# Kernel optimization log

Hardware: AMD Instinct MI355X
Metric: run time of the kernel (lower is better)

## Reference

```python
import jax, jax.numpy as jnp
import numpy as np

D_STATE = 16
D_CONV = 4


def layer_norm(x, g, b, eps=1e-5):
    mu = jnp.mean(x, axis=-1, keepdims=True)
    var = jnp.mean(jnp.square(x - mu), axis=-1, keepdims=True)
    return (x - mu) * jax.lax.rsqrt(var + eps) * g + b


def silu(x):
    return x * jax.nn.sigmoid(x)


def mamba(x, in_w, conv_w, conv_b, xproj_w, dt_w, dt_b, Alog, Dp, out_w):
    # x: [B, L, d_model]; in_w: [2*di, d_model]; conv_w: [di, d_conv]
    Bsz, L, _ = x.shape
    di = Dp.shape[0]
    xz = jnp.einsum('bld,ed->ble', x, in_w)          # [B,L,2*di]
    xs, z = jnp.split(xz, 2, axis=-1)
    # causal depthwise conv over L
    xt = xs.transpose(0, 2, 1)                        # [B,di,L]
    xt = jax.lax.conv_general_dilated(
        xt, conv_w[:, None, :], (1,), [(D_CONV - 1, 0)],
        feature_group_count=di, dimension_numbers=('NCH', 'OIH', 'NCH'))
    xs = silu((xt + conv_b[None, :, None]).transpose(0, 2, 1))  # [B,L,di]
    # input-dependent dt, B, C
    dbl = jnp.einsum('bld,ed->ble', xs, xproj_w)      # [B,L,dt_rank+2*ds]
    dt_rank = dt_w.shape[1]
    dt, Bc, Cc = jnp.split(dbl, [dt_rank, dt_rank + D_STATE], axis=-1)
    dt = jax.nn.softplus(jnp.einsum('blr,dr->bld', dt, dt_w) + dt_b)  # [B,L,di]
    A = -jnp.exp(Alog)                                # [di,ds]
    dA = jnp.exp(dt[..., None] * A)                   # [B,L,di,ds]
    dBx = dt[..., None] * Bc[:, :, None, :] * xs[..., None]  # [B,L,di,ds]

    def step(h, inp):
        dA_t, dBx_t, C_t = inp                        # [B,di,ds],[B,di,ds],[B,ds]
        h = dA_t * h + dBx_t
        y = jnp.einsum('bds,bs->bd', h, C_t)
        return h, y

    h0 = jnp.zeros((Bsz, di, D_STATE), x.dtype)
    _, ys = jax.lax.scan(step, h0, (dA.transpose(1, 0, 2, 3),
                                    dBx.transpose(1, 0, 2, 3),
                                    Cc.transpose(1, 0, 2)))
    y = ys.transpose(1, 0, 2) + Dp * xs               # [B,L,di]
    y = y * silu(z)
    return jnp.einsum('bld,od->blo', y, out_w)        # [B,L,d_model]


def _make_mamba_params(key, d_model, scale=0.02):
    di = 2 * d_model
    dt_rank = (d_model + 15) // 16
    ks = jax.random.split(key, 7)
    in_w = jax.random.normal(ks[0], (2 * di, d_model), jnp.float32) * scale
    conv_w = jax.random.normal(ks[1], (di, D_CONV), jnp.float32) * scale
    conv_b = jnp.zeros((di,), jnp.float32)
    xproj_w = jax.random.normal(ks[2], (dt_rank + 2 * D_STATE, di), jnp.float32) * scale
    dt_w = jax.random.normal(ks[3], (di, dt_rank), jnp.float32) * scale
    dt_b = jax.random.uniform(ks[4], (di,), jnp.float32, -5.0, -2.0)
    Alog = jnp.log(jnp.tile(jnp.arange(1, D_STATE + 1, dtype=jnp.float32), (di, 1)))
    Dp = jnp.ones((di,), jnp.float32)
    out_w = jax.random.normal(ks[5], (d_model, di), jnp.float32) * scale
    return in_w, conv_w, conv_b, xproj_w, dt_w, dt_b, Alog, Dp, out_w


def setup_inputs() -> dict:
    key = jax.random.key(0)
    B, L, D = 4, 2048, 1024
    DFF = 4 * D
    ks = jax.random.split(key, 8)
    x = jax.random.normal(ks[0], (B, L, D), jnp.float32)
    m1 = _make_mamba_params(ks[1], D)
    m2 = _make_mamba_params(ks[2], D)
    names1 = ['m1_in_w', 'm1_conv_w', 'm1_conv_b', 'm1_xproj_w', 'm1_dt_w', 'm1_dt_b', 'm1_Alog', 'm1_D', 'm1_out_w']
    names2 = ['m2_in_w', 'm2_conv_w', 'm2_conv_b', 'm2_xproj_w', 'm2_dt_w', 'm2_dt_b', 'm2_Alog', 'm2_D', 'm2_out_w']
    inp = {'x': x}
    inp.update(dict(zip(names1, m1)))
    inp.update(dict(zip(names2, m2)))
    inp['norm_g'] = jnp.ones((D,), jnp.float32)
    inp['norm_b'] = jnp.zeros((D,), jnp.float32)
    inp['ffn_g'] = jnp.ones((D,), jnp.float32)
    inp['ffn_b'] = jnp.zeros((D,), jnp.float32)
    inp['ff1_w'] = jax.random.normal(ks[3], (DFF, D), jnp.float32) * 0.02
    inp['ff1_b'] = jnp.zeros((DFF,), jnp.float32)
    inp['ff2_w'] = jax.random.normal(ks[4], (D, DFF), jnp.float32) * 0.02
    inp['ff2_b'] = jnp.zeros((D,), jnp.float32)
    return inp


def reference(x,
              m1_in_w, m1_conv_w, m1_conv_b, m1_xproj_w, m1_dt_w, m1_dt_b, m1_Alog, m1_D, m1_out_w,
              m2_in_w, m2_conv_w, m2_conv_b, m2_xproj_w, m2_dt_w, m2_dt_b, m2_Alog, m2_D, m2_out_w,
              norm_g, norm_b, ffn_g, ffn_b, ff1_w, ff1_b, ff2_w, ff2_b):
    # BiDirectionalAddBlock (dropout/droppath = identity in eval)
    h = layer_norm(x, norm_g, norm_b)
    fwd = mamba(h, m1_in_w, m1_conv_w, m1_conv_b, m1_xproj_w, m1_dt_w, m1_dt_b, m1_Alog, m1_D, m1_out_w)
    bwd = mamba(h[:, ::-1], m2_in_w, m2_conv_w, m2_conv_b, m2_xproj_w, m2_dt_w, m2_dt_b, m2_Alog, m2_D, m2_out_w)
    block_out = jax.nn.gelu(fwd + bwd + x, approximate=False)  # note: original does NOT flip bwd back
    x = x + block_out
    # FeedForward
    hf = layer_norm(x, ffn_g, ffn_b)
    hf = jax.nn.gelu(jnp.einsum('bld,hd->blh', hf, ff1_w) + ff1_b, approximate=False)
    x = x + jnp.einsum('blh,dh->bld', hf, ff2_w) + ff2_b
    return x
```

## Files before the change

### kernel.cpp

```cpp
#include <hip/hip_runtime.h>
#include <cmath>


namespace {

using u16 = unsigned short;
using uint = unsigned int;

constexpr int kB = 4;
constexpr int kL = 2048;
constexpr int kD = 1024;
constexpr int kDI = 2048;
constexpr int kDFF = 4096;
constexpr int kDS = 16;
constexpr int kDtRank = 64;
constexpr int kNPad = 128;
constexpr int kM = kB * kL;
constexpr int kNCH = 64;

typedef short bf16x8 __attribute__((ext_vector_type(8)));
typedef float f32x4  __attribute__((ext_vector_type(4)));
typedef unsigned short ushort8 __attribute__((ext_vector_type(8)));

__device__ __forceinline__ float bf2f(u16 u) {
  union { unsigned int i; float f; } c; c.i = ((unsigned int)u) << 16; return c.f;
}
__device__ __forceinline__ u16 f2bf(float f) {
  union { float f; unsigned int i; } c; c.f = f;
  return (u16)((c.i + 0x7FFFu + ((c.i >> 16) & 1u)) >> 16);
}
__device__ __forceinline__ float geluf(float v) {
  return 0.5f * v * (1.f + erff(v * 0.70710678118654752f));
}
__device__ __forceinline__ float softplusf(float v) {
  return (v > 0.f) ? (v + log1pf(__expf(-v))) : log1pf(__expf(v));
}
__device__ __forceinline__ float siluf(float v) {
  return v / (1.f + __expf(-v));
}
__device__ __forceinline__ float exp2_fast(float v) {
  return __builtin_amdgcn_exp2f(v);
}
__device__ __forceinline__ float softplus_fast(float v) {
  const float a = __builtin_fabsf(v);
  const float e = exp2_fast(-a * 1.44269504088896f);
  const float l = __log2f(1.f + e) * 0.69314718055995f;
  return fmaxf(v, 0.f) + l;
}

__device__ __forceinline__ void async16(const u16* g, u16* l) {
  __builtin_amdgcn_global_load_lds(
      (const __attribute__((address_space(1))) uint*)g,
      (__attribute__((address_space(3))) uint*)l, 16, 0, 0);
}

__global__ __launch_bounds__(256) void ln_kernel(
    const float* __restrict__ x, const float* __restrict__ g,
    const float* __restrict__ b, u16* __restrict__ out) {
  const int row = blockIdx.x;
  const int tid = threadIdx.x;
  const float4 v = ((const float4*)(x + (size_t)row * kD))[tid];
  float s  = v.x + v.y + v.z + v.w;
  float ss = v.x * v.x + v.y * v.y + v.z * v.z + v.w * v.w;
  #pragma unroll
  for (int off = 32; off; off >>= 1) {
    s  += __shfl_xor(s, off);
    ss += __shfl_xor(ss, off);
  }
  __shared__ float ls[4], lss[4];
  const int wid = tid >> 6;
  if ((tid & 63) == 0) { ls[wid] = s; lss[wid] = ss; }
  __syncthreads();
  s  = ls[0] + ls[1] + ls[2] + ls[3];
  ss = lss[0] + lss[1] + lss[2] + lss[3];
  const float mu  = s * (1.f / kD);
  const float inv = rsqrtf(ss * (1.f / kD) - mu * mu + 1e-5f);
  const float4 gg = ((const float4*)g)[tid];
  const float4 bb = ((const float4*)b)[tid];
  ushort4 o;
  o.x = f2bf((v.x - mu) * inv * gg.x + bb.x);
  o.y = f2bf((v.y - mu) * inv * gg.y + bb.y);
  o.z = f2bf((v.z - mu) * inv * gg.z + bb.z);
  o.w = f2bf((v.w - mu) * inv * gg.w + bb.w);
  ((ushort4*)(out + (size_t)row * kD))[tid] = o;
}

__global__ __launch_bounds__(256) void combine_ln_kernel(
    const float* __restrict__ x, float* __restrict__ out,
    const float* __restrict__ g, const float* __restrict__ b,
    u16* __restrict__ h) {
  const int row = blockIdx.x;
  const int tid = threadIdx.x;
  const float4 xv = ((const float4*)(x + (size_t)row * kD))[tid];
  const float4 bv = ((const float4*)(out + (size_t)row * kD))[tid];
  float4 o;
  o.x = xv.x + geluf(bv.x + xv.x);
  o.y = xv.y + geluf(bv.y + xv.y);
  o.z = xv.z + geluf(bv.z + xv.z);
  o.w = xv.w + geluf(bv.w + xv.w);
  ((float4*)(out + (size_t)row * kD))[tid] = o;
  float s  = o.x + o.y + o.z + o.w;
  float ss = o.x * o.x + o.y * o.y + o.z * o.z + o.w * o.w;
  #pragma unroll
  for (int off = 32; off; off >>= 1) {
    s  += __shfl_xor(s, off);
    ss += __shfl_xor(ss, off);
  }
  __shared__ float ls[4], lss[4];
  const int wid = tid >> 6;
  if ((tid & 63) == 0) { ls[wid] = s; lss[wid] = ss; }
  __syncthreads();
  s  = ls[0] + ls[1] + ls[2] + ls[3];
  ss = lss[0] + lss[1] + lss[2] + lss[3];
  const float mu  = s * (1.f / kD);
  const float inv = rsqrtf(ss * (1.f / kD) - mu * mu + 1e-5f);
  const float4 gg = ((const float4*)g)[tid];
  const float4 bb = ((const float4*)b)[tid];
  ushort4 ho;
  ho.x = f2bf((o.x - mu) * inv * gg.x + bb.x);
  ho.y = f2bf((o.y - mu) * inv * gg.y + bb.y);
  ho.z = f2bf((o.z - mu) * inv * gg.z + bb.z);
  ho.w = f2bf((o.w - mu) * inv * gg.w + bb.w);
  ((ushort4*)(h + (size_t)row * kD))[tid] = ho;
}

struct KJob { const float* s; u16* d; int n4; int blk0; int xp; };
struct KJobs { KJob j[10]; };

__global__ __launch_bounds__(256) void cvt_all_kernel(KJobs J) {
  const int bi = blockIdx.x;
  #pragma unroll
  for (int k = 0; k < 10; k++) {
    const KJob job = J.j[k];
    const int nb = (job.n4 + 255) >> 8;
    if (bi >= job.blk0 && bi < job.blk0 + nb) {
      const int i = (bi - job.blk0) * 256 + threadIdx.x;
      if (i < job.n4) {
        ushort4 o = {0, 0, 0, 0};
        bool valid = true;
        if (job.xp) valid = ((i * 4) >> 11) < (kDtRank + 2 * kDS);
        if (valid) {
          const float4 v = ((const float4*)job.s)[i];
          o.x = f2bf(v.x); o.y = f2bf(v.y); o.z = f2bf(v.z); o.w = f2bf(v.w);
        }
        ((ushort4*)job.d)[i] = o;
      }
      return;
    }
  }
}

template <int TILEN, int ACT, bool BIAS, bool ACC, bool OUTBF, bool REV,
          bool AMAP, bool CMAP>
__global__ __launch_bounds__(256) void gemm_mfma(
    const u16* __restrict__ A, int lda,
    const u16* __restrict__ W, int ldw,
    void* __restrict__ Cp, int ldc, int K,
    const float* __restrict__ bias, int seg_len, int row_off) {
  constexpr int MI = (TILEN == 128) ? 4 : 2;
  constexpr int WSTR = TILEN / 32;
  __shared__ __align__(16) u16 As[128][64];
  __shared__ __align__(16) u16 Ws[TILEN][64];
  const int tid  = threadIdx.x;
  const int bm   = blockIdx.x * 128;
  const int bn   = blockIdx.y * TILEN;
  const int lane = tid & 63;
  const int wv   = tid >> 6;
  const int wm   = (TILEN == 128) ? (wv >> 1) * 64 : wv * 32;
  const int wn   = (TILEN == 128) ? (wv & 1) * 64 : 0;
  const int l15  = lane & 15;
  const int quad = lane >> 4;
  const int srow = lane >> 3;
  const int swz  = ((lane & 7) ^ srow) * 8;
  const int jx   = (l15 & 7) * 16;

  int ab = 0, all0 = bm;
  if (AMAP || CMAP) {
    ab = bm / seg_len;
    all0 = bm - ab * seg_len;
  }

  int arowv[4];
  #pragma unroll
  for (int it = 0; it < 4; it++) {
    const int rl = it * 32 + wv * 8 + srow;
    if (AMAP) {
      arowv[it] = REV ? (ab * kL + kL - 1 - row_off - all0 - rl)
                      : (ab * kL + row_off + all0 + rl);
    } else {
      arowv[it] = bm + rl;
    }
  }

  f32x4 acc[MI][4];
  #pragma unroll
  for (int i = 0; i < MI; i++)
    #pragma unroll
    for (int j = 0; j < 4; j++) acc[i][j] = (f32x4){0.f, 0.f, 0.f, 0.f};

  for (int k0 = 0; k0 < K; k0 += 64) {
    #pragma unroll
    for (int it = 0; it < 4; it++) {
      const int rl = it * 32 + wv * 8 + srow;
      async16(A + (size_t)arowv[it] * lda + k0 + swz, &As[it * 32 + wv * 8][0]);
    }
    #pragma unroll
    for (int it = 0; it < WSTR; it++) {
      const int rl = it * 32 + wv * 8 + srow;
      async16(W + (size_t)(bn + rl) * ldw + k0 + swz, &Ws[it * 32 + wv * 8][0]);
    }
    __syncthreads();
    #pragma unroll
    for (int ks = 0; ks < 64; ks += 32) {
      const int cb = ((ks >> 3) + quad) * 16;
      bf16x8 af[MI], wf[4];
      #pragma unroll
      for (int i = 0; i < MI; i++)
        af[i] = *(const bf16x8*)((const char*)&As[wm + i * 16 + l15][0] +
                                 (cb ^ jx));
      #pragma unroll
      for (int j = 0; j < 4; j++)
        wf[j] = *(const bf16x8*)((const char*)&Ws[wn + j * 16 + l15][0] +
                                 (cb ^ jx));
      #pragma unroll
      for (int i = 0; i < MI; i++)
        #pragma unroll
        for (int j = 0; j < 4; j++)
          acc[i][j] = __builtin_amdgcn_mfma_f32_16x16x32_bf16(
              af[i], wf[j], acc[i][j], 0, 0, 0);
    }
    __syncthreads();
  }

  #pragma unroll
  for (int i = 0; i < MI; i++) {
    #pragma unroll
    for (int j = 0; j < 4; j++) {
      const int col = bn + wn + j * 16 + l15;
      #pragma unroll
      for (int r = 0; r < 4; r++) {
        const int rl2 = wm + i * 16 + quad * 4 + r;
        const int crow = CMAP ? (ab * kL + row_off + all0 + rl2) : (bm + rl2);
        float v = acc[i][j][r];
        if (BIAS) v += bias[col];
        if (ACT == 1) v = softplusf(v);
        if (ACT == 2) v = geluf(v);
        if (OUTBF) {
          ((u16*)Cp)[(size_t)crow * ldc + col] = f2bf(v);
        } else {
          float* p = (float*)Cp + (size_t)crow * ldc + col;
          if (ACC) *p = *p + v; else *p = v;
        }
      }
    }
  }
}

__global__ __launch_bounds__(256) void dt_kernel(
    const u16* __restrict__ dbl, const u16* __restrict__ wdt,
    const float* __restrict__ bias, u16* __restrict__ dtb) {
  __shared__ __align__(16) u16 sh[2][128][64];
  const int tid  = threadIdx.x;
  const int bm   = blockIdx.x * 128;
  const int bn   = blockIdx.y * 128;
  const int lane = tid & 63;
  const int wv   = tid >> 6;
  const int wm   = (wv >> 1) * 64;
  const int wn   = (wv & 1) * 64;
  const int l15  = lane & 15;
  const int quad = lane >> 4;
  const int srow = lane >> 3;
  const int swz  = ((lane & 7) ^ srow) * 8;
  const int jx   = (l15 & 7) * 16;

  #pragma unroll
  for (int it = 0; it < 4; it++) {
    const int rl = it * 32 + wv * 8 + srow;
    async16(dbl + (size_t)(bm + rl) * kNPad + swz, &sh[0][it * 32 + wv * 8][0]);
    async16(wdt + (size_t)(bn + rl) * kDtRank + swz,
            &sh[1][it * 32 + wv * 8][0]);
  }
  __syncthreads();

  f32x4 acc[4][4];
  #pragma unroll
  for (int i = 0; i < 4; i++)
    #pragma unroll
    for (int j = 0; j < 4; j++) acc[i][j] = (f32x4){0.f, 0.f, 0.f, 0.f};

  #pragma unroll
  for (int ks = 0; ks < 2; ks++) {
    const int cb = (ks * 4 + quad) * 16;
    bf16x8 af[4], wf[4];
    #pragma unroll
    for (int i = 0; i < 4; i++)
      af[i] = *(const bf16x8*)((const char*)&sh[0][wm + i * 16 + l15][0] +
                               (cb ^ jx));
    #pragma unroll
    for (int j = 0; j < 4; j++)
      wf[j] = *(const bf16x8*)((const char*)&sh[1][wn + j * 16 + l15][0] +
                               (cb ^ jx));
    #pragma unroll
    for (int i = 0; i < 4; i++)
      #pragma unroll
      for (int j = 0; j < 4; j++)
        acc[i][j] = __builtin_amdgcn_mfma_f32_16x16x32_bf16(
            af[i], wf[j], acc[i][j], 0, 0, 0);
  }
  __syncthreads();

  u16* C = &sh[0][0][0];
  #pragma unroll
  for (int i = 0; i < 4; i++) {
    #pragma unroll
    for (int j = 0; j < 4; j++) {
      const int colL = wn + j * 16 + l15;
      const float bv = bias[bn + colL];
      #pragma unroll
      for (int r = 0; r < 4; r++) {
        const int rl2 = wm + i * 16 + quad * 4 + r;
        C[rl2 * 128 + colL] = f2bf(softplus_fast(acc[i][j][r] + bv));
      }
    }
  }
  __syncthreads();

  #pragma unroll
  for (int i = 0; i < 8; i++) {
    const int cidx = i * 256 + tid;
    const int row  = cidx >> 4;
    const int cin  = (cidx & 15) * 8;
    const ushort8 val = *(const ushort8*)&C[row * 128 + cin];
    *(ushort8*)&dtb[(size_t)(bm + row) * kDI + bn + cin] = val;
  }
}

__global__ __launch_bounds__(256) void conv_silu_kernel(
    const u16* __restrict__ xz, const float* __restrict__ w,
    const float* __restrict__ cb, u16* __restrict__ xs,
    const u16* __restrict__ tail_in, u16* __restrict__ tail_out,
    int seg_len, int row_off) {
  const int t = blockIdx.x * 256 + threadIdx.x;
  const int c = t & (kDI - 1);
  const int r = t >> 11;
  const int b = r / seg_len;
  const int ll = r - b * seg_len;
  const int tpos = row_off + ll;

  const float xv0 = bf2f(xz[(size_t)r * (2 * kDI) + c]);
  float acc = cb[c] + w[c * 4 + 3] * xv0;
  #pragma unroll
  for (int j = 1; j <= 3; j++) {
    if (tpos - j >= 0) {
      float xp;
      if (ll - j >= 0) {
        xp = bf2f(xz[(size_t)(r - j) * (2 * kDI) + c]);
      } else {
        xp = bf2f(tail_in[(b * 3 + (3 + ll - j)) * kDI + c]);
      }
      acc += w[c * 4 + 3 - j] * xp;
    }
  }
  xs[(size_t)r * kDI + c] = f2bf(siluf(acc));
  if (ll >= seg_len - 3) {
    tail_out[(b * 3 + (ll - (seg_len - 3))) * kDI + c] = f2bf(xv0);
  }
}

__global__ __launch_bounds__(256, 8) void scan_phaseA(
    const u16* __restrict__ dt, const u16* __restrict__ xs,
    const u16* __restrict__ dbl, const float* __restrict__ Alog,
    float* __restrict__ Pbuf, float* __restrict__ Hbuf,
    int Lseg, int Lc) {
  __shared__ float Bls[32][16];
  const int tid = threadIdx.x;
  const int c = blockIdx.x * 256 + tid;
  const int k = blockIdx.y;
  const int b = blockIdx.z;
  const int base = b * Lseg + k * Lc;
  for (int idx = tid; idx < Lc * 16; idx += 256) {
    const int r = idx >> 4, j = idx & 15;
    Bls[r][j] = bf2f(dbl[(size_t)(base + r) * kNPad + kDtRank + j]);
  }
  __syncthreads();
  float Ac[16], h[16];
  float dtsum = 0.f;
  #pragma unroll
  for (int s = 0; s < 16; s++) {
    Ac[s] = -__expf(Alog[c * kDS + s]) * 1.44269504088896f;
    h[s] = 0.f;
  }
  for (int r = 0; r < Lc; r++) {
    const size_t row = (size_t)(base + r);
    const float dtv = bf2f(dt[row * kDI + c]);
    const float dtx = dtv * bf2f(xs[row * kDI + c]);
    dtsum += dtv;
    const float4* Brow = (const float4*)Bls[r];
    #pragma unroll
    for (int s4 = 0; s4 < 4; s4++) {
      const float4 Bv = Brow[s4];
      const float bb[4] = {Bv.x, Bv.y, Bv.z, Bv.w};
      #pragma unroll
      for (int q = 0; q < 4; q++) {
        const int s = s4 * 4 + q;
        const float dA = exp2_fast(dtv * Ac[s]);
        h[s] = dA * h[s] + dtx * bb[q];
      }
    }
  }
  const size_t o = (((size_t)b * kNCH + k) * kDI + c) * 16;
  #pragma unroll
  for (int s4 = 0; s4 < 4; s4++) {
    *(float4*)&Pbuf[o + s4 * 4] =
        make_float4(exp2_fast(Ac[s4 * 4 + 0] * dtsum),
                    exp2_fast(Ac[s4 * 4 + 1] * dtsum),
                    exp2_fast(Ac[s4 * 4 + 2] * dtsum),
                    exp2_fast(Ac[s4 * 4 + 3] * dtsum));
    *(float4*)&Hbuf[o + s4 * 4] =
        make_float4(h[s4 * 4], h[s4 * 4 + 1], h[s4 * 4 + 2], h[s4 * 4 + 3]);
  }
}

__global__ __launch_bounds__(256) void scan_phaseB(
    float* __restrict__ Pbuf, const float* __restrict__ Hbuf,
    float* __restrict__ hstate, int first) {
  const int t = blockIdx.x * 256 + threadIdx.x;
  const int s = t & 15;
  const int c = (t >> 4) & (kDI - 1);
  const int b = t >> 15;
  float cur = first ? 0.f : hstate[t];
  for (int k = 0; k < kNCH; k++) {
    const size_t idx = (((size_t)b * kNCH + k) * kDI + c) * 16 + s;
    const float p = Pbuf[idx];
    const float hl = Hbuf[idx];
    Pbuf[idx] = cur;
    cur = p * cur + hl;
  }
  hstate[t] = cur;
}

__global__ __launch_bounds__(256, 8) void scan_phaseC(
    const u16* __restrict__ dt, u16* __restrict__ xs,
    const u16* __restrict__ dbl, const u16* __restrict__ xz,
    const float* __restrict__ Alog, const float* __restrict__ Dp,
    const float* __restrict__ Pbuf, int Lseg, int Lc) {
  __shared__ float BC[32][32];
  const int tid = threadIdx.x;
  const int c = blockIdx.x * 256 + tid;
  const int k = blockIdx.y;
  const int b = blockIdx.z;
  const int base = b * Lseg + k * Lc;
  for (int idx = tid; idx < Lc * 32; idx += 256) {
    const int r = idx >> 5, j = idx & 31;
    BC[r][j] = bf2f(dbl[(size_t)(base + r) * kNPad + kDtRank + j]);
  }
  __syncthreads();
  float Ac[16], h[16];
  const size_t o = (((size_t)b * kNCH + k) * kDI + c) * 16;
  #pragma unroll
  for (int s4 = 0; s4 < 4; s4++) {
    const float4 hv = *(const float4*)&Pbuf[o + s4 * 4];
    h[s4 * 4 + 0] = hv.x; h[s4 * 4 + 1] = hv.y;
    h[s4 * 4 + 2] = hv.z; h[s4 * 4 + 3] = hv.w;
  }
  #pragma unroll
  for (int s = 0; s < 16; s++)
    Ac[s] = -__expf(Alog[c * kDS + s]) * 1.44269504088896f;
  const float Dv = Dp[c];
  for (int r = 0; r < Lc; r++) {
    const size_t row = (size_t)(base + r);
    const float dtv = bf2f(dt[row * kDI + c]);
    const float xv = bf2f(xs[row * kDI + c]);
    const float dtx = dtv * xv;
    float y = 0.f;
    const float4* Brow = (const float4*)BC[r];
    const float4* Crow = (const float4*)&BC[r][16];
    #pragma unroll
    for (int s4 = 0; s4 < 4; s4++) {
      const float4 Bv = Brow[s4];
      const float4 Cv = Crow[s4];
      const float bb[4] = {Bv.x, Bv.y, Bv.z, Bv.w};
      const float cc[4] = {Cv.x, Cv.y, Cv.z, Cv.w};
      #pragma unroll
      for (int q = 0; q < 4; q++) {
        const int s = s4 * 4 + q;
        const float dA = exp2_fast(dtv * Ac[s]);
        h[s] = dA * h[s] + dtx * bb[q];
        y += h[s] * cc[q];
      }
    }
    const float z = bf2f(xz[row * (2 * kDI) + kDI + c]);
    xs[row * kDI + c] = f2bf((y + Dv * xv) * siluf(z));
  }
}

}

extern "C" void kernel_launch(void* const* d_in, const int* in_sizes, int n_in,
                              void* d_out, int out_size, void* d_ws,
                              size_t ws_size, hipStream_t stream) {
  const float* x = (const float*)d_in[0];
  const float* in_w[2]    = {(const float*)d_in[1],  (const float*)d_in[10]};
  const float* conv_w[2]  = {(const float*)d_in[2],  (const float*)d_in[11]};
  const float* conv_b[2]  = {(const float*)d_in[3],  (const float*)d_in[12]};
  const float* xproj_w[2] = {(const float*)d_in[4],  (const float*)d_in[13]};
  const float* dt_w[2]    = {(const float*)d_in[5],  (const float*)d_in[14]};
  const float* dt_b[2]    = {(const float*)d_in[6],  (const float*)d_in[15]};
  const float* Alog[2]    = {(const float*)d_in[7],  (const float*)d_in[16]};
  const float* Dp[2]      = {(const float*)d_in[8],  (const float*)d_in[17]};
  const float* out_w[2]   = {(const float*)d_in[9],  (const float*)d_in[18]};
  const float* norm_g = (const float*)d_in[19];
  const float* norm_b = (const float*)d_in[20];
  const float* ffn_g  = (const float*)d_in[21];
  const float* ffn_b  = (const float*)d_in[22];
  const float* ff1_w  = (const float*)d_in[23];
  const float* ff1_b  = (const float*)d_in[24];
  const float* ff2_w  = (const float*)d_in[25];
  const float* ff2_b  = (const float*)d_in[26];
  float* out = (float*)d_out;

  constexpr size_t kWCache =
      2 * ((size_t)4096 * kD + (size_t)kD * kDI + (size_t)kNPad * kDI +
           (size_t)kDI * kDtRank) * 2 +
      ((size_t)kDFF * kD + (size_t)kD * kDFF) * 2;
  auto need = [](int nseg) -> size_t {
    const size_t mseg = (size_t)kM / nseg;
    size_t sz = kWCache + 4096;
    sz += (size_t)kM * kD * 2;
    sz += mseg * 4096 * 2;
    sz += mseg * 2048 * 2;
    sz += mseg * 128 * 2;
    sz += mseg * 2048 * 2;
    sz += 2 * (size_t)kB * kNCH * kDI * kDS * 4;
    sz += (size_t)kB * kDI * kDS * 4;
    sz += 2 * (size_t)kB * 3 * kDI * 2;
    sz += 32 * 256;
    return sz;
  };
  int nseg = 1;
  while (nseg <= 16 && need(nseg) > ws_size) nseg *= 2;
  if (nseg > 16) return;
  const int Lseg = kL / nseg;
  const int Mseg = kM / nseg;
  const int Lc = Lseg / kNCH;

  char* base = (char*)d_ws;
  size_t off = 0;
  auto alloc = [&](size_t bytes) {
    char* p = base + off;
    off = (off + bytes + 255) & ~(size_t)255;
    return p;
  };
  u16* w_in[2], *w_out[2], *w_xp[2], *w_dt[2];
  for (int m = 0; m < 2; m++) {
    w_in[m]  = (u16*)alloc((size_t)4096 * kD * 2);
    w_out[m] = (u16*)alloc((size_t)kD * kDI * 2);
    w_xp[m]  = (u16*)alloc((size_t)kNPad * kDI * 2);
    w_dt[m]  = (u16*)alloc((size_t)kDI * kDtRank * 2);
  }
  u16* w_f1 = (u16*)alloc((size_t)kDFF * kD * 2);
  u16* w_f2 = (u16*)alloc((size_t)kD * kDFF * 2);
  u16*   h      = (u16*)alloc((size_t)kM * kD * 2);
  u16*   xz     = (u16*)alloc((size_t)Mseg * 4096 * 2);
  u16*   xs     = (u16*)alloc((size_t)Mseg * 2048 * 2);
  u16*   dbl    = (u16*)alloc((size_t)Mseg * 128 * 2);
  u16*   dtb    = (u16*)alloc((size_t)Mseg * 2048 * 2);
  float* Pbuf   = (float*)alloc((size_t)kB * kNCH * kDI * kDS * 4);
  float* Hbuf   = (float*)alloc((size_t)kB * kNCH * kDI * kDS * 4);
  float* hstate = (float*)alloc((size_t)kB * kDI * kDS * 4);
  u16*   tail0  = (u16*)alloc((size_t)kB * 3 * kDI * 2);
  u16*   tail1  = (u16*)alloc((size_t)kB * 3 * kDI * 2);

  {
    KJobs J;
    int b = 0, ji = 0;
    auto addjob = [&](const float* s, u16* d, int n4, int xp) {
      J.j[ji].s = s; J.j[ji].d = d; J.j[ji].n4 = n4;
      J.j[ji].blk0 = b; J.j[ji].xp = xp;
      b += (n4 + 255) >> 8;
      ji++;
    };
    for (int m = 0; m < 2; m++) {
      addjob(in_w[m],  w_in[m],  (4096 * kD) / 4, 0);
      addjob(out_w[m], w_out[m], (kD * kDI) / 4, 0);
      addjob(xproj_w[m], w_xp[m], (kNPad * kDI) / 4, 1);
      addjob(dt_w[m],  w_dt[m],  (kDI * kDtRank) / 4, 0);
    }
    addjob(ff1_w, w_f1, (kDFF * kD) / 4, 0);
    addjob(ff2_w, w_f2, (kD * kDFF) / 4, 0);
    cvt_all_kernel<<<b, 256, 0, stream>>>(J);
  }

  ln_kernel<<<kM, 256, 0, stream>>>(x, norm_g, norm_b, h);

  for (int m = 0; m < 2; m++) {
    for (int s = 0; s < nseg; s++) {
      const int l0 = s * Lseg;
      u16* tin  = (s & 1) ? tail0 : tail1;
      u16* tout = (s & 1) ? tail1 : tail0;
      if (m == 0)
        gemm_mfma<128, 0, false, false, true, false, true, false>
            <<<dim3(Mseg / 128, 4096 / 128), 256, 0, stream>>>(
                h, kD, w_in[m], kD, xz, 4096, kD, nullptr, Lseg, l0);
      else
        gemm_mfma<128, 0, false, false, true, true, true, false>
            <<<dim3(Mseg / 128, 4096 / 128), 256, 0, stream>>>(
                h, kD, w_in[m], kD, xz, 4096, kD, nullptr, Lseg, l0);
      conv_silu_kernel<<<(Mseg * kDI) / 256, 256, 0, stream>>>(
          xz, conv_w[m], conv_b[m], xs, tin, tout, Lseg, l0);
      gemm_mfma<128, 0, false, false, true, false, false, false>
          <<<dim3(Mseg / 128, 1), 256, 0, stream>>>(
              xs, kDI, w_xp[m], kDI, dbl, kNPad, kDI, nullptr, Lseg, l0);
      dt_kernel<<<dim3(Mseg / 128, kDI / 128), 256, 0, stream>>>(
          dbl, w_dt[m], dt_b[m], dtb);
      scan_phaseA<<<dim3(kDI / 256, kNCH, kB), 256, 0, stream>>>(
          dtb, xs, dbl, Alog[m], Pbuf, Hbuf, Lseg, Lc);
      scan_phaseB<<<(kB * kDI * kDS) / 256, 256, 0, stream>>>(
          Pbuf, Hbuf, hstate, (s == 0) ? 1 : 0);
      scan_phaseC<<<dim3(kDI / 256, kNCH, kB), 256, 0, stream>>>(
          dtb, xs, dbl, xz, Alog[m], Dp[m], Pbuf, Lseg, Lc);
      if (m == 0)
        gemm_mfma<64, 0, false, false, false, false, false, true>
            <<<dim3(Mseg / 128, kD / 64), 256, 0, stream>>>(
                xs, kDI, w_out[m], kDI, out, kD, kDI, nullptr, Lseg, l0);
      else
        gemm_mfma<64, 0, false, true, false, false, false, true>
            <<<dim3(Mseg / 128, kD / 64), 256, 0, stream>>>(
                xs, kDI, w_out[m], kDI, out, kD, kDI, nullptr, Lseg, l0);
    }
  }

  combine_ln_kernel<<<kM, 256, 0, stream>>>(x, out, ffn_g, ffn_b, h);

  for (int s = 0; s < nseg; s++) {
    const int r0 = s * Mseg;
    gemm_mfma<128, 2, true, false, true, false, true, false>
        <<<dim3(Mseg / 128, kDFF / 128), 256, 0, stream>>>(
            h, kD, w_f1, kD, xz, kDFF, kD, ff1_b, Mseg, r0);
    gemm_mfma<64, 0, true, true, false, false, false, true>
        <<<dim3(Mseg / 128, kD / 64), 256, 0, stream>>>(
            xz, kDFF, w_f2, kDFF, out, kD, kDFF, ff2_b, Mseg, r0);
  }
}
```

Baseline: 1.231 ms.

## Split-K the x-projection GEMM and add XCD-aware block swizzle to GEMMs

The x-projection GEMM (N=128, K=2048) previously ran with only Mseg/128 blocks. It is now split into 8 K-slices that write fp32 partials, followed by a reduce kernel that sums them and converts to bf16, which raises parallelism. All other GEMMs gain a block-index remap that places consecutive tiles on the same XCD for better L2 reuse on MI355X. The cost is an extra fp32 partial buffer, more workspace, and one additional kernel launch per segment.

```diff
diff --git a/kernel.cpp b/kernel.cpp
--- a/kernel.cpp
+++ b/kernel.cpp
@@ -151,7 +151,7 @@
 }
 
 template <int TILEN, int ACT, bool BIAS, bool ACC, bool OUTBF, bool REV,
-          bool AMAP, bool CMAP>
+          bool AMAP, bool CMAP, bool XSWZ>
 __global__ __launch_bounds__(256) void gemm_mfma(
     const u16* __restrict__ A, int lda,
     const u16* __restrict__ W, int ldw,
@@ -162,8 +162,17 @@
   __shared__ __align__(16) u16 As[128][64];
   __shared__ __align__(16) u16 Ws[TILEN][64];
   const int tid  = threadIdx.x;
-  const int bm   = blockIdx.x * 128;
-  const int bn   = blockIdx.y * TILEN;
+  int bx = blockIdx.x, by = blockIdx.y;
+  if (XSWZ) {
+    const int nbx = gridDim.x;
+    const int nwg = nbx * gridDim.y;
+    const int bid = by * nbx + bx;
+    const int sbid = (bid & 7) * (nwg >> 3) + (bid >> 3);
+    bx = sbid % nbx;
+    by = sbid / nbx;
+  }
+  const int bm   = bx * 128;
+  const int bn   = by * TILEN;
   const int lane = tid & 63;
   const int wv   = tid >> 6;
   const int wm   = (TILEN == 128) ? (wv >> 1) * 64 : wv * 32;
@@ -254,6 +263,85 @@
       }
     }
   }
+}
+
+__global__ __launch_bounds__(256) void xproj_k8_kernel(
+    const u16* __restrict__ A, const u16* __restrict__ W,
+    float* __restrict__ xpp, int Mrows) {
+  __shared__ __align__(16) u16 As[128][64];
+  __shared__ __align__(16) u16 Ws[128][64];
+  const int tid  = threadIdx.x;
+  const int bm   = blockIdx.x * 128;
+  const int kq   = blockIdx.y;
+  const int lane = tid & 63;
+  const int wv   = tid >> 6;
+  const int wm   = (wv >> 1) * 64;
+  const int wn   = (wv & 1) * 64;
+  const int l15  = lane & 15;
+  const int quad = lane >> 4;
+  const int srow = lane >> 3;
+  const int swz  = ((lane & 7) ^ srow) * 8;
+  const int jx   = (l15 & 7) * 16;
+
+  f32x4 acc[4][4];
+  #pragma unroll
+  for (int i = 0; i < 4; i++)
+    #pragma unroll
+    for (int j = 0; j < 4; j++) acc[i][j] = (f32x4){0.f, 0.f, 0.f, 0.f};
+
+  const int kbeg = kq * 256;
+  for (int k0 = kbeg; k0 < kbeg + 256; k0 += 64) {
+    #pragma unroll
+    for (int it = 0; it < 4; it++) {
+      const int rl = it * 32 + wv * 8 + srow;
+      async16(A + (size_t)(bm + rl) * kDI + k0 + swz, &As[it * 32 + wv * 8][0]);
+      async16(W + (size_t)rl * kDI + k0 + swz, &Ws[it * 32 + wv * 8][0]);
+    }
+    __syncthreads();
+    #pragma unroll
+    for (int ks = 0; ks < 64; ks += 32) {
+      const int cb = ((ks >> 3) + quad) * 16;
+      bf16x8 af[4], wf[4];
+      #pragma unroll
+      for (int i = 0; i < 4; i++)
+        af[i] = *(const bf16x8*)((const char*)&As[wm + i * 16 + l15][0] +
+                                 (cb ^ jx));
+      #pragma unroll
+      for (int j = 0; j < 4; j++)
+        wf[j] = *(const bf16x8*)((const char*)&Ws[wn + j * 16 + l15][0] +
+                                 (cb ^ jx));
+      #pragma unroll
+      for (int i = 0; i < 4; i++)
+        #pragma unroll
+        for (int j = 0; j < 4; j++)
+          acc[i][j] = __builtin_amdgcn_mfma_f32_16x16x32_bf16(
+              af[i], wf[j], acc[i][j], 0, 0, 0);
+    }
+    __syncthreads();
+  }
+
+  float* outp = xpp + (size_t)kq * Mrows * kNPad;
+  #pragma unroll
+  for (int i = 0; i < 4; i++) {
+    #pragma unroll
+    for (int j = 0; j < 4; j++) {
+      const int col = wn + j * 16 + l15;
+      #pragma unroll
+      for (int r = 0; r < 4; r++) {
+        const int row = bm + wm + i * 16 + quad * 4 + r;
+        outp[(size_t)row * kNPad + col] = acc[i][j][r];
+      }
+    }
+  }
+}
+
+__global__ __launch_bounds__(256) void xproj_reduce_kernel(
+    const float* __restrict__ xpp, u16* __restrict__ dbl, int n) {
+  const int i = blockIdx.x * 256 + threadIdx.x;
+  float s = 0.f;
+  #pragma unroll
+  for (int k = 0; k < 8; k++) s += xpp[(size_t)k * n + i];
+  dbl[i] = f2bf(s);
 }
 
 __global__ __launch_bounds__(256) void dt_kernel(
@@ -531,6 +619,7 @@
     sz += mseg * 2048 * 2;
     sz += mseg * 128 * 2;
     sz += mseg * 2048 * 2;
+    sz += 8 * mseg * 128 * 4;
     sz += 2 * (size_t)kB * kNCH * kDI * kDS * 4;
     sz += (size_t)kB * kDI * kDS * 4;
     sz += 2 * (size_t)kB * 3 * kDI * 2;
@@ -565,6 +654,7 @@
   u16*   xs     = (u16*)alloc((size_t)Mseg * 2048 * 2);
   u16*   dbl    = (u16*)alloc((size_t)Mseg * 128 * 2);
   u16*   dtb    = (u16*)alloc((size_t)Mseg * 2048 * 2);
+  float* xpp    = (float*)alloc((size_t)8 * Mseg * 128 * 4);
   float* Pbuf   = (float*)alloc((size_t)kB * kNCH * kDI * kDS * 4);
   float* Hbuf   = (float*)alloc((size_t)kB * kNCH * kDI * kDS * 4);
   float* hstate = (float*)alloc((size_t)kB * kDI * kDS * 4);
@@ -599,18 +689,19 @@
       u16* tin  = (s & 1) ? tail0 : tail1;
       u16* tout = (s & 1) ? tail1 : tail0;
       if (m == 0)
-        gemm_mfma<128, 0, false, false, true, false, true, false>
+        gemm_mfma<128, 0, false, false, true, false, true, false, true>
             <<<dim3(Mseg / 128, 4096 / 128), 256, 0, stream>>>(
                 h, kD, w_in[m], kD, xz, 4096, kD, nullptr, Lseg, l0);
       else
-        gemm_mfma<128, 0, false, false, true, true, true, false>
+        gemm_mfma<128, 0, false, false, true, true, true, false, true>
             <<<dim3(Mseg / 128, 4096 / 128), 256, 0, stream>>>(
                 h, kD, w_in[m], kD, xz, 4096, kD, nullptr, Lseg, l0);
       conv_silu_kernel<<<(Mseg * kDI) / 256, 256, 0, stream>>>(
           xz, conv_w[m], conv_b[m], xs, tin, tout, Lseg, l0);
-      gemm_mfma<128, 0, false, false, true, false, false, false>
-          <<<dim3(Mseg / 128, 1), 256, 0, stream>>>(
-              xs, kDI, w_xp[m], kDI, dbl, kNPad, kDI, nullptr, Lseg, l0);
+      xproj_k8_kernel<<<dim3(Mseg / 128, 8), 256, 0, stream>>>(
+          xs, w_xp[m], xpp, Mseg);
+      xproj_reduce_kernel<<<(Mseg * kNPad) / 256, 256, 0, stream>>>(
+          xpp, dbl, Mseg * kNPad);
       dt_kernel<<<dim3(Mseg / 128, kDI / 128), 256, 0, stream>>>(
           dbl, w_dt[m], dt_b[m], dtb);
       scan_phaseA<<<dim3(kDI / 256, kNCH, kB), 256, 0, stream>>>(
@@ -620,11 +711,11 @@
       scan_phaseC<<<dim3(kDI / 256, kNCH, kB), 256, 0, stream>>>(
           dtb, xs, dbl, xz, Alog[m], Dp[m], Pbuf, Lseg, Lc);
       if (m == 0)
-        gemm_mfma<64, 0, false, false, false, false, false, true>
+        gemm_mfma<64, 0, false, false, false, false, false, true, true>
             <<<dim3(Mseg / 128, kD / 64), 256, 0, stream>>>(
                 xs, kDI, w_out[m], kDI, out, kD, kDI, nullptr, Lseg, l0);
       else
-        gemm_mfma<64, 0, false, true, false, false, false, true>
+        gemm_mfma<64, 0, false, true, false, false, false, true, true>
             <<<dim3(Mseg / 128, kD / 64), 256, 0, stream>>>(
                 xs, kDI, w_out[m], kDI, out, kD, kDI, nullptr, Lseg, l0);
     }
@@ -634,10 +725,10 @@
 
   for (int s = 0; s < nseg; s++) {
     const int r0 = s * Mseg;
-    gemm_mfma<128, 2, true, false, true, false, true, false>
+    gemm_mfma<128, 2, true, false, true, false, true, false, true>
         <<<dim3(Mseg / 128, kDFF / 128), 256, 0, stream>>>(
             h, kD, w_f1, kD, xz, kDFF, kD, ff1_b, Mseg, r0);
-    gemm_mfma<64, 0, true, true, false, false, false, true>
+    gemm_mfma<64, 0, true, true, false, false, false, true, true>
         <<<dim3(Mseg / 128, kD / 64), 256, 0, stream>>>(
             xz, kDFF, w_f2, kDFF, out, kD, kDFF, ff2_b, Mseg, r0);
   }
```

Measured after the change: 1.528 ms. 1.24x slower.
